# Kernel optimization log

Hardware: AMD Instinct MI355X
Metric: run time of the kernel (lower is better)

## Reference

```python
import jax, jax.numpy as jnp
import numpy as np

N_HEADS = 16
NEG_INF = float('-inf')


def setup_inputs() -> dict:
    key = jax.random.key(0)
    ks = jax.random.split(key, 8)
    B, S, D = 8, 1024, 1024
    inp = {
        'q': jax.random.normal(ks[0], (B, S, D), jnp.float32),
        'k': jax.random.normal(ks[1], (B, S, D), jnp.float32),
        'v': jax.random.normal(ks[2], (B, S, D), jnp.float32),
        'key_padding_mask': jnp.zeros((B, S), bool),
        'Wq': jax.random.normal(ks[3], (D, D), jnp.float32) / np.sqrt(D),
        'bq': jnp.zeros((D,), jnp.float32),
        'Wk': jax.random.normal(ks[4], (D, D), jnp.float32) / np.sqrt(D),
        'bk': jnp.zeros((D,), jnp.float32),
        'Wv': jax.random.normal(ks[5], (D, D), jnp.float32) / np.sqrt(D),
        'bv': jnp.zeros((D,), jnp.float32),
        'Wo': jax.random.normal(ks[6], (D, D), jnp.float32) / np.sqrt(D),
        'bo': jnp.zeros((D,), jnp.float32),
    }
    return inp


def reference(q, k, v, key_padding_mask, Wq, bq, Wk, bk, Wv, bv, Wo, bo):
    B, T, D = q.shape
    S = k.shape[1]
    H = N_HEADS
    dh = D // H
    causal = True

    # projections (torch Linear: x @ W.T + b)
    qh = (q @ Wq.T + bq).reshape(B, T, H, dh).transpose(0, 2, 1, 3)  # b h t d
    kh = (k @ Wk.T + bk).reshape(B, S, H, dh).transpose(0, 2, 1, 3)  # b h s d
    vh = (v @ Wv.T + bv).reshape(B, S, H, dh).transpose(0, 2, 1, 3)  # b h s d

    s = jnp.einsum('bhtd,bhsd->bhts', qh, kh) / jnp.sqrt(jnp.asarray(dh, s_dtype(qh)))
    s = jnp.where(key_padding_mask[:, None, None, :], NEG_INF, s)
    if causal:
        cmask = jnp.triu(jnp.full((T, S), NEG_INF, s.dtype), 1)
        s = s + cmask[None, None]
    a = jax.nn.softmax(s.astype(jnp.float32), axis=-1).astype(s.dtype)
    o = jnp.einsum('bhts,bhsd->bhtd', a, vh)
    o = o.transpose(0, 2, 1, 3).reshape(B, T, D)
    return o @ Wo.T + bo


def s_dtype(x):
    return x.dtype
```

## Files before the change

### kernel.cpp

```cpp
#include <hip/hip_runtime.h>
#include <hip/hip_bf16.h>

typedef unsigned short u16;
typedef unsigned int u32;
typedef __attribute__((ext_vector_type(8))) short bf16x8;
typedef __attribute__((ext_vector_type(4))) float f32x4;

#define LOG2E 1.44269504088896340736f
#define QSCALE (0.125f * LOG2E)
#define DEFER_THR 8.0f


__device__ inline u16 f2bf(float f) {
  union { float f; u32 u; } v; v.f = f;
  u32 r = v.u + 0x7fffu + ((v.u >> 16) & 1u);
  return (u16)(r >> 16);
}

__device__ inline void gload_lds16(const void* g, void* l) {
  __builtin_amdgcn_global_load_lds(
      (const __attribute__((address_space(1))) u32*)g,
      (__attribute__((address_space(3))) u32*)l, 16, 0, 0);
}

template<int CTRL>
__device__ inline float dppmov(float x) {
  int i = __builtin_bit_cast(int, x);
  int r = __builtin_amdgcn_update_dpp(i, i, CTRL, 0xf, 0xf, false);
  return __builtin_bit_cast(float, r);
}
__device__ inline float rowmax16(float v) {
  v = fmaxf(v, dppmov<0x128>(v));
  v = fmaxf(v, dppmov<0x124>(v));
  v = fmaxf(v, dppmov<0x122>(v));
  v = fmaxf(v, dppmov<0x121>(v));
  return v;
}
__device__ inline float rowsum16(float v) {
  v += dppmov<0x128>(v);
  v += dppmov<0x124>(v);
  v += dppmov<0x122>(v);
  v += dppmov<0x121>(v);
  return v;
}


__global__ void cvt_multi(const float4* __restrict__ s0, const float4* __restrict__ s1,
                          const float4* __restrict__ s2, const float4* __restrict__ s3,
                          ushort4* __restrict__ d0, ushort4* __restrict__ d1,
                          ushort4* __restrict__ d2, ushort4* __restrict__ d3, int n4) {
  const float4* s; ushort4* d;
  switch (blockIdx.y) {
    case 0: s = s0; d = d0; break;
    case 1: s = s1; d = d1; break;
    case 2: s = s2; d = d2; break;
    default: s = s3; d = d3; break;
  }
  int stride = gridDim.x * blockDim.x;
  for (int i = blockIdx.x * blockDim.x + threadIdx.x; i < n4; i += stride) {
    float4 v = s[i];
    ushort4 o;
    o.x = f2bf(v.x); o.y = f2bf(v.y); o.z = f2bf(v.z); o.w = f2bf(v.w);
    d[i] = o;
  }
}


__global__ void mask_flags(const unsigned char* __restrict__ mask,
                           unsigned char* __restrict__ flags) {
  int t = threadIdx.x;
  if (t >= 128) return;
  const uint4* p = (const uint4*)(mask + (size_t)t * 64);
  uint4 a = p[0], b = p[1], c = p[2], d = p[3];
  u32 v = a.x | a.y | a.z | a.w | b.x | b.y | b.z | b.w |
          c.x | c.y | c.z | c.w | d.x | d.y | d.z | d.w;
  flags[t] = v ? 1 : 0;
}


#define GATE() do { \
    asm volatile("s_waitcnt vmcnt(4)" ::: "memory"); \
    __builtin_amdgcn_s_barrier(); \
    __builtin_amdgcn_sched_barrier(0); \
  } while (0)

#define READ_A(buf, qm)                                                        \
  do {                                                                         \
    const char* base_ = (const char*)&sA[buf][wm][0];                          \
    _Pragma("unroll")                                                          \
    for (int fi = 0; fi < 4; ++fi) {                                           \
      _Pragma("unroll")                                                        \
      for (int kk = 0; kk < 2; ++kk) {                                         \
        int row_ = (qm) * 64 + fi * 16 + r;                                    \
        int j_ = kk * 4 + g;                                                   \
        af[fi][kk] = *(const bf16x8*)(base_ + row_ * 128 +                     \
                                      ((j_ ^ (row_ & 7)) << 4));               \
      }                                                                        \
    }                                                                          \
  } while (0)

#define READ_B(buf, qn, BF)                                                    \
  do {                                                                         \
    const char* base_ = (const char*)&sB[buf][wn >> 1][0];                     \
    _Pragma("unroll")                                                          \
    for (int fj = 0; fj < 2; ++fj) {                                           \
      _Pragma("unroll")                                                        \
      for (int kk = 0; kk < 2; ++kk) {                                         \
        int row_ = (wn & 1) * 64 + (qn) * 32 + fj * 16 + r;                    \
        int j_ = kk * 4 + g;                                                   \
        BF[fj][kk] = *(const bf16x8*)(base_ + row_ * 128 +                     \
                                      ((j_ ^ (row_ & 7)) << 4));               \
      }                                                                        \
    }                                                                          \
  } while (0)

#define MFMA8(qm, qn, BF)                                                      \
  do {                                                                         \
    __builtin_amdgcn_s_setprio(1);                                             \
    _Pragma("unroll")                                                          \
    for (int kk = 0; kk < 2; ++kk) {                                           \
      _Pragma("unroll")                                                        \
      for (int fi = 0; fi < 4; ++fi) {                                         \
        _Pragma("unroll")                                                      \
        for (int fj = 0; fj < 2; ++fj) {                                       \
          acc[(qm) * 4 + fi][(qn) * 2 + fj] =                                  \
              __builtin_amdgcn_mfma_f32_16x16x32_bf16(                         \
                  af[fi][kk], BF[fj][kk], acc[(qm) * 4 + fi][(qn) * 2 + fj],   \
                  0, 0, 0);                                                    \
        }                                                                      \
      }                                                                        \
    }                                                                          \
    __builtin_amdgcn_s_setprio(0);                                             \
  } while (0)

__global__ __launch_bounds__(512) void gemm_qkv8(
    const u16* __restrict__ Aq, const u16* __restrict__ Ak, const u16* __restrict__ Av,
    const u16* __restrict__ Wqb, const u16* __restrict__ Wkb, const u16* __restrict__ Wvb,
    const float* __restrict__ bqp, const float* __restrict__ bkp, const float* __restrict__ bvp,
    u16* __restrict__ Qh, u16* __restrict__ Kh, u16* __restrict__ Vt,
    int M, int N, int K) {
  __shared__ u16 sA[2][2][128 * 64];
  __shared__ u16 sB[2][2][128 * 64];

  const int hw = blockIdx.z * 128 + blockIdx.y * 4 + blockIdx.x;
  const int lg = (hw & 7) * 48 + (hw >> 3);
  const int z = lg >> 7;
  const int rem = lg & 127;
  const int m0 = (rem >> 2) * 256;
  const int n0 = (rem & 3) * 256;

  const u16* A  = (z == 0) ? Aq : (z == 1) ? Ak : Av;
  const u16* Bt = (z == 0) ? Wqb : (z == 1) ? Wkb : Wvb;
  const float* bias = (z == 0) ? bqp : (z == 1) ? bkp : bvp;

  const int tid = threadIdx.x;
  const int lane = tid & 63;
  const int wave = tid >> 6;
  const int g = lane >> 4;
  const int r = lane & 15;
  const int wm = wave >> 2;
  const int wn = wave & 3;

  f32x4 acc[8][4] = {};
  bf16x8 af[4][2], bf0[2][2], bf1[2][2];

  auto stageA = [&](int buf, int half, int kt) {
    const int k0 = kt * 64;
#pragma unroll
    for (int i = 0; i < 2; ++i) {
      int c = tid + i * 512;
      int row = c >> 3, cc = c & 7;
      gload_lds16(A + (size_t)(m0 + half * 128 + row) * K + k0 + ((cc ^ (row & 7)) * 8),
                  &sA[buf][half][0] + c * 8);
    }
  };
  auto stageB = [&](int buf, int half, int kt) {
    const int k0 = kt * 64;
#pragma unroll
    for (int i = 0; i < 2; ++i) {
      int c = tid + i * 512;
      int row = c >> 3, cc = c & 7;
      gload_lds16(Bt + (size_t)(n0 + half * 128 + row) * K + k0 + ((cc ^ (row & 7)) * 8),
                  &sB[buf][half][0] + c * 8);
    }
  };

  const int NT = K / 64;

  stageB(0, 0, 0); stageB(0, 1, 0); stageA(0, 0, 0); stageA(0, 1, 0);
  stageB(1, 0, 1); stageA(1, 0, 1);
  asm volatile("s_waitcnt vmcnt(0)" ::: "memory");
  __builtin_amdgcn_s_barrier();
  __builtin_amdgcn_sched_barrier(0);

  for (int t = 0; t < NT; ++t) {
    const int buf = t & 1;
    READ_A(buf, 0);
    READ_B(buf, 0, bf0);
    if (t + 1 < NT) stageB(buf ^ 1, 1, t + 1);
    GATE();
    MFMA8(0, 0, bf0);
    READ_B(buf, 1, bf1);
    if (t + 1 < NT) stageA(buf ^ 1, 1, t + 1);
    GATE();
    MFMA8(0, 1, bf1);
    READ_A(buf, 1);
    if (t + 2 < NT) stageB(buf, 0, t + 2);
    GATE();
    MFMA8(1, 0, bf0);
    if (t + 2 < NT) stageA(buf, 0, t + 2);
    GATE();
    MFMA8(1, 1, bf1);
  }

#pragma unroll
  for (int fi = 0; fi < 8; ++fi) {
    int rowb = m0 + wm * 128 + fi * 16 + g * 4;
#pragma unroll
    for (int fj = 0; fj < 4; ++fj) {
      int col = n0 + wn * 64 + fj * 16 + r;
      float bv = bias[col];
#pragma unroll
      for (int q = 0; q < 4; ++q) {
        int row = rowb + q;
        float v = acc[fi][fj][q] + bv;
        int b = row >> 10, t = row & 1023, h = col >> 6, d = col & 63;
        if (z == 0) {
          Qh[((((size_t)b * 16 + h) << 10) + t) * 64 + d] = f2bf(v * QSCALE);
        } else if (z == 1) {
          Kh[((((size_t)b * 16 + h) << 10) + t) * 64 + d] = f2bf(v);
        } else {
          Vt[(((size_t)b * 16 + h) * 64 + d) * 1024 + t] = f2bf(v);
        }
      }
    }
  }
}


__global__ __launch_bounds__(256) void gemm_o(
    const u16* __restrict__ A, const u16* __restrict__ Bt,
    const float* __restrict__ bias, float* __restrict__ Cout,
    int M, int N, int K) {
  constexpr int BK = 32;
  __shared__ u16 sA[2][128 * BK];
  __shared__ u16 sB[2][128 * BK];

  const int hw = blockIdx.y * 8 + blockIdx.x;
  const int lg = (hw & 7) * 64 + (hw >> 3);
  const int m0 = (lg >> 3) * 128;
  const int n0 = (lg & 7) * 128;

  const int tid = threadIdx.x;
  const int lane = tid & 63;
  const int wave = tid >> 6;
  const int g = lane >> 4;
  const int r = lane & 15;
  const int wr = wave >> 1, wc = wave & 1;

  f32x4 acc[4][4] = {};

  auto stage = [&](int buf, int kt) {
    const int k0 = kt * BK;
#pragma unroll
    for (int i = 0; i < 2; ++i) {
      int c = tid + i * 256;
      int row = c >> 2, cc = c & 3;
      gload_lds16(A + (size_t)(m0 + row) * K + k0 + cc * 8, &sA[buf][0] + c * 8);
    }
#pragma unroll
    for (int i = 0; i < 2; ++i) {
      int c = tid + i * 256;
      int row = c >> 2, cc = c & 3;
      gload_lds16(Bt + (size_t)(n0 + row) * K + k0 + cc * 8, &sB[buf][0] + c * 8);
    }
  };

  stage(0, 0);
  const int NT = K / BK;
  for (int kt = 0; kt < NT; ++kt) {
    __syncthreads();
    if (kt + 1 < NT) stage((kt + 1) & 1, kt + 1);
    const u16* a_base = &sA[kt & 1][0];
    const u16* b_base = &sB[kt & 1][0];
    bf16x8 avf[4], bvf[4];
#pragma unroll
    for (int i = 0; i < 4; ++i) {
      avf[i] = *(const bf16x8*)(a_base + (wr * 64 + i * 16 + r) * BK + g * 8);
      bvf[i] = *(const bf16x8*)(b_base + (wc * 64 + i * 16 + r) * BK + g * 8);
    }
#pragma unroll
    for (int i = 0; i < 4; ++i)
#pragma unroll
      for (int j = 0; j < 4; ++j)
        acc[i][j] = __builtin_amdgcn_mfma_f32_16x16x32_bf16(avf[i], bvf[j], acc[i][j], 0, 0, 0);
  }

#pragma unroll
  for (int i = 0; i < 4; ++i) {
    int rowb = m0 + wr * 64 + i * 16 + g * 4;
#pragma unroll
    for (int j = 0; j < 4; ++j) {
      int col = n0 + wc * 64 + j * 16 + r;
      float bv = bias[col];
#pragma unroll
      for (int q = 0; q < 4; ++q) {
        int row = rowb + q;
        Cout[(size_t)row * N + col] = acc[i][j][q] + bv;
      }
    }
  }
}


__global__ __launch_bounds__(256) void attn_fwd(
    const u16* __restrict__ Qh, const u16* __restrict__ Kh,
    const u16* __restrict__ Vt, const unsigned char* __restrict__ mask,
    const unsigned char* __restrict__ padflags,
    u16* __restrict__ O) {
  constexpr int S = 1024, DH = 64;
  __shared__ u16 sK[2][64 * 64];
  __shared__ u16 sV[2][64 * 64];
  __shared__ u16 sP[4][16 * 64];

  const int tid = threadIdx.x, lane = tid & 63, wave = tid >> 6;
  const int g = lane >> 4, r = lane & 15;
  const int bh = blockIdx.x;
  const int qt = (int)gridDim.y - 1 - (int)blockIdx.y;
  const int b = bh >> 4, h = bh & 15;
  const int qw = qt * 128 + wave * 32;

  bf16x8 qf[2][2];
#pragma unroll
  for (int u = 0; u < 2; ++u) {
    const u16* Qb = Qh + ((size_t)bh * S + qw + u * 16 + r) * DH;
    qf[u][0] = *(const bf16x8*)(Qb + g * 8);
    qf[u][1] = *(const bf16x8*)(Qb + 32 + g * 8);
  }

  f32x4 acc[2][4] = {};
  float mrun[2][4], lrun[2][4];
#pragma unroll
  for (int u = 0; u < 2; ++u)
#pragma unroll
    for (int i = 0; i < 4; ++i) { mrun[u][i] = -INFINITY; lrun[u][i] = 0.f; }

  auto stage = [&](int buf, int kvt) {
    const int s0k = kvt * 64;
#pragma unroll
    for (int i = 0; i < 2; ++i) {
      int c = tid + i * 256;
      int row = c >> 3;
      int cc = (c & 7) ^ (row & 7);
      gload_lds16(Kh + ((size_t)bh * S + s0k + row) * DH + cc * 8, &sK[buf][0] + c * 8);
      gload_lds16(Vt + ((size_t)bh * DH + row) * S + s0k + cc * 8, &sV[buf][0] + c * 8);
    }
  };

  const int NT = 2 * (qt + 1);
  stage(0, 0);
  for (int kvt = 0; kvt < NT; ++kvt) {
    __syncthreads();
    if (kvt + 1 < NT) stage((kvt + 1) & 1, kvt + 1);
    const int cur = kvt & 1;
    const int s0 = kvt * 64;
    const bool pad = padflags[b * 16 + (s0 >> 6)] != 0;
    const u16* Kb = &sK[cur][0];
    const u16* Vb = &sV[cur][0];
    u16* Pw = &sP[wave][0];

#pragma unroll
    for (int u = 0; u < 2; ++u) {
      const int qg = qw + u * 16;
      if (s0 > qg + 15) continue;
      const bool diag = (s0 + 63 > qg);

      f32x4 sc[4] = {};
      __builtin_amdgcn_s_setprio(1);
#pragma unroll
      for (int ss = 0; ss < 4; ++ss) {
#pragma unroll
        for (int kc = 0; kc < 2; ++kc) {
          int krow = ss * 16 + r;
          int byteoff = krow * 128 + kc * 64 + g * 16;
          bf16x8 kf = *(const bf16x8*)((const char*)Kb + (byteoff ^ ((krow & 7) << 4)));
          sc[ss] = __builtin_amdgcn_mfma_f32_16x16x32_bf16(qf[u][kc], kf, sc[ss], 0, 0, 0);
        }
      }
      __builtin_amdgcn_s_setprio(0);

      float sv[4][4];
      float pmax[4] = {-INFINITY, -INFINITY, -INFINITY, -INFINITY};
#pragma unroll
      for (int ss = 0; ss < 4; ++ss) {
        float padd = 0.f;
        if (pad) {
          int s_g = s0 + ss * 16 + r;
          if (mask[(size_t)b * S + s_g]) padd = -INFINITY;
        }
#pragma unroll
        for (int reg = 0; reg < 4; ++reg) {
          float v = sc[ss][reg] + padd;
          if (diag) {
            int s_g = s0 + ss * 16 + r;
            int q_g = qg + g * 4 + reg;
            if (s_g > q_g) v = -INFINITY;
          }
          sv[ss][reg] = v;
          pmax[reg] = fmaxf(pmax[reg], v);
        }
      }

      float tm[4];
#pragma unroll
      for (int reg = 0; reg < 4; ++reg) tm[reg] = rowmax16(pmax[reg]);
      float dmax = fmaxf(fmaxf(tm[0] - mrun[u][0], tm[1] - mrun[u][1]),
                         fmaxf(tm[2] - mrun[u][2], tm[3] - mrun[u][3]));
      if (__any(dmax > DEFER_THR)) {
#pragma unroll
        for (int reg = 0; reg < 4; ++reg) {
          float newm = fmaxf(mrun[u][reg], tm[reg]);
          float alpha = (newm == -INFINITY) ? 1.f : exp2f(mrun[u][reg] - newm);
          mrun[u][reg] = newm;
          float rs = 0.f;
#pragma unroll
          for (int ss = 0; ss < 4; ++ss) {
            float p = (newm == -INFINITY) ? 0.f : exp2f(sv[ss][reg] - newm);
            sv[ss][reg] = p;
            rs += p;
          }
          rs = rowsum16(rs);
          lrun[u][reg] = lrun[u][reg] * alpha + rs;
#pragma unroll
          for (int df = 0; df < 4; ++df) acc[u][df][reg] *= alpha;
        }
      } else {
#pragma unroll
        for (int reg = 0; reg < 4; ++reg) {
          float m = mrun[u][reg];
          float rs = 0.f;
#pragma unroll
          for (int ss = 0; ss < 4; ++ss) {
            float p = (m == -INFINITY) ? 0.f : exp2f(sv[ss][reg] - m);
            sv[ss][reg] = p;
            rs += p;
          }
          rs = rowsum16(rs);
          lrun[u][reg] += rs;
        }
      }

#pragma unroll
      for (int ss = 0; ss < 4; ++ss) {
#pragma unroll
        for (int reg = 0; reg < 4; ++reg) {
          int qrow = g * 4 + reg;
          int byteoff = qrow * 128 + (ss * 16 + r) * 2;
          u32 bits = __builtin_bit_cast(u32, sv[ss][reg]);
          *(u16*)((char*)Pw + (byteoff ^ ((qrow & 7) << 4))) = (u16)(bits >> 16);
        }
      }

      __builtin_amdgcn_s_setprio(1);
#pragma unroll
      for (int sc2 = 0; sc2 < 2; ++sc2) {
        int pbyte = r * 128 + sc2 * 64 + g * 16;
        bf16x8 pf = *(const bf16x8*)((const char*)Pw + (pbyte ^ ((r & 7) << 4)));
#pragma unroll
        for (int df = 0; df < 4; ++df) {
          int vrow = df * 16 + r;
          int vbyte = vrow * 128 + sc2 * 64 + g * 16;
          bf16x8 vf = *(const bf16x8*)((const char*)Vb + (vbyte ^ ((vrow & 7) << 4)));
          acc[u][df] = __builtin_amdgcn_mfma_f32_16x16x32_bf16(pf, vf, acc[u][df], 0, 0, 0);
        }
      }
      __builtin_amdgcn_s_setprio(0);
    }
  }

#pragma unroll
  for (int u = 0; u < 2; ++u) {
#pragma unroll
    for (int reg = 0; reg < 4; ++reg) {
      float l = lrun[u][reg];
      float inv = (l > 0.f) ? 1.f / l : 0.f;
      int t = qw + u * 16 + g * 4 + reg;
#pragma unroll
      for (int df = 0; df < 4; ++df) {
        float vo = acc[u][df][reg] * inv;
        O[((size_t)b * 1024 + t) * 1024 + h * 64 + df * 16 + r] = f2bf(vo);
      }
    }
  }
}


extern "C" void kernel_launch(void* const* d_in, const int* in_sizes, int n_in,
                              void* d_out, int out_size, void* d_ws, size_t ws_size,
                              hipStream_t stream) {
  const float* q  = (const float*)d_in[0];
  const float* k  = (const float*)d_in[1];
  const float* v  = (const float*)d_in[2];
  const unsigned char* mask = (const unsigned char*)d_in[3];
  const float* Wq = (const float*)d_in[4];
  const float* bq = (const float*)d_in[5];
  const float* Wk = (const float*)d_in[6];
  const float* bk = (const float*)d_in[7];
  const float* Wv = (const float*)d_in[8];
  const float* bv = (const float*)d_in[9];
  const float* Wo = (const float*)d_in[10];
  const float* bo = (const float*)d_in[11];

  const int M = 8192, N = 1024, K = 1024;
  const size_t MB = 1u << 20;
  char* ws = (char*)d_ws;

  u16* Aq   = (u16*)(ws);
  u16* Ak   = (u16*)(ws + 16 * MB);
  u16* Av   = (u16*)(ws + 32 * MB);
  u16* Qh   = (u16*)(ws + 48 * MB);
  u16* Kh   = (u16*)(ws + 64 * MB);
  u16* Vt   = (u16*)(ws + 80 * MB);
  u16* Wqb  = (u16*)(ws + 96 * MB);
  u16* Wkb  = Wqb + (1u << 20);
  u16* Wvb  = Wkb + (1u << 20);
  u16* Wob  = Wvb + (1u << 20);
  unsigned char* flags = (unsigned char*)(ws + 104 * MB);
  u16* AttO = Aq;

  cvt_multi<<<dim3(1024, 3), 256, 0, stream>>>(
      (const float4*)q, (const float4*)k, (const float4*)v, (const float4*)q,
      (ushort4*)Aq, (ushort4*)Ak, (ushort4*)Av, (ushort4*)Aq, (M * K) / 4);
  cvt_multi<<<dim3(256, 4), 256, 0, stream>>>(
      (const float4*)Wq, (const float4*)Wk, (const float4*)Wv, (const float4*)Wo,
      (ushort4*)Wqb, (ushort4*)Wkb, (ushort4*)Wvb, (ushort4*)Wob, (N * K) / 4);
  mask_flags<<<1, 128, 0, stream>>>(mask, flags);

  gemm_qkv8<<<dim3(4, 32, 3), 512, 0, stream>>>(
      Aq, Ak, Av, Wqb, Wkb, Wvb, bq, bk, bv, Qh, Kh, Vt, M, N, K);

  attn_fwd<<<dim3(128, 8), 256, 0, stream>>>(Qh, Kh, Vt, mask, flags, AttO);

  gemm_o<<<dim3(8, 64), 256, 0, stream>>>(
      AttO, Wob, bo, (float*)d_out, M, N, K);
}
```

Before: 241.5 us.

## Shrink QKV GEMM tile to 256x128 and merge conversion launches

The QKV projection GEMM tile shrinks from 256x256 to 256x128. Its eight waves are rearranged as 4x2, each owning a 64x64 sub-tile, and the grid doubles to 768 blocks for better occupancy and fewer partial waves across the CUs. The vmcnt waits are moved so there is one explicit wait per k-step instead of a wait at every barrier. The activation and weight fp32-to-bf16 conversion kernels are merged into a single launch. In exchange, each tile reuses its A data less, and the reworked wait counts risk race conditions if the outstanding-load accounting is off.

```diff
diff --git a/kernel.cpp b/kernel.cpp
--- a/kernel.cpp
+++ b/kernel.cpp
@@ -45,22 +45,30 @@
 }
 
 
-__global__ void cvt_multi(const float4* __restrict__ s0, const float4* __restrict__ s1,
-                          const float4* __restrict__ s2, const float4* __restrict__ s3,
-                          ushort4* __restrict__ d0, ushort4* __restrict__ d1,
-                          ushort4* __restrict__ d2, ushort4* __restrict__ d3, int n4) {
-  const float4* s; ushort4* d;
+__global__ void cvt_all(const float4* __restrict__ q, const float4* __restrict__ k,
+                        const float4* __restrict__ v,
+                        const float4* __restrict__ Wq, const float4* __restrict__ Wk,
+                        const float4* __restrict__ Wv, const float4* __restrict__ Wo,
+                        ushort4* __restrict__ dq, ushort4* __restrict__ dk,
+                        ushort4* __restrict__ dv,
+                        ushort4* __restrict__ dWq, ushort4* __restrict__ dWk,
+                        ushort4* __restrict__ dWv, ushort4* __restrict__ dWo,
+                        int n4A, int n4W) {
+  const float4* s; ushort4* d; int n4;
   switch (blockIdx.y) {
-    case 0: s = s0; d = d0; break;
-    case 1: s = s1; d = d1; break;
-    case 2: s = s2; d = d2; break;
-    default: s = s3; d = d3; break;
+    case 0: s = q;  d = dq;  n4 = n4A; break;
+    case 1: s = k;  d = dk;  n4 = n4A; break;
+    case 2: s = v;  d = dv;  n4 = n4A; break;
+    case 3: s = Wq; d = dWq; n4 = n4W; break;
+    case 4: s = Wk; d = dWk; n4 = n4W; break;
+    case 5: s = Wv; d = dWv; n4 = n4W; break;
+    default: s = Wo; d = dWo; n4 = n4W; break;
   }
   int stride = gridDim.x * blockDim.x;
   for (int i = blockIdx.x * blockDim.x + threadIdx.x; i < n4; i += stride) {
-    float4 v = s[i];
+    float4 x = s[i];
     ushort4 o;
-    o.x = f2bf(v.x); o.y = f2bf(v.y); o.z = f2bf(v.z); o.w = f2bf(v.w);
+    o.x = f2bf(x.x); o.y = f2bf(x.y); o.z = f2bf(x.z); o.w = f2bf(x.w);
     d[i] = o;
   }
 }
@@ -78,54 +86,53 @@
 }
 
 
-#define GATE() do { \
-    asm volatile("s_waitcnt vmcnt(4)" ::: "memory"); \
+#define BAR8() do { \
     __builtin_amdgcn_s_barrier(); \
     __builtin_amdgcn_sched_barrier(0); \
   } while (0)
 
-#define READ_A(buf, qm)                                                        \
+#define READ_A8(buf, qm)                                                       \
   do {                                                                         \
-    const char* base_ = (const char*)&sA[buf][wm][0];                          \
+    const char* ab_ = (const char*)&sA[buf][wm >> 1][0];                       \
     _Pragma("unroll")                                                          \
-    for (int fi = 0; fi < 4; ++fi) {                                           \
+    for (int fi = 0; fi < 2; ++fi) {                                           \
       _Pragma("unroll")                                                        \
       for (int kk = 0; kk < 2; ++kk) {                                         \
-        int row_ = (qm) * 64 + fi * 16 + r;                                    \
+        int row_ = (wm & 1) * 64 + (qm) * 32 + fi * 16 + r;                    \
         int j_ = kk * 4 + g;                                                   \
-        af[fi][kk] = *(const bf16x8*)(base_ + row_ * 128 +                     \
+        af[fi][kk] = *(const bf16x8*)(ab_ + row_ * 128 +                       \
                                       ((j_ ^ (row_ & 7)) << 4));               \
       }                                                                        \
     }                                                                          \
   } while (0)
 
-#define READ_B(buf, qn, BF)                                                    \
+#define READ_B8(buf, qn, BF)                                                   \
   do {                                                                         \
-    const char* base_ = (const char*)&sB[buf][wn >> 1][0];                     \
+    const char* bb_ = (const char*)&sB[buf][wn][0];                            \
     _Pragma("unroll")                                                          \
     for (int fj = 0; fj < 2; ++fj) {                                           \
       _Pragma("unroll")                                                        \
       for (int kk = 0; kk < 2; ++kk) {                                         \
-        int row_ = (wn & 1) * 64 + (qn) * 32 + fj * 16 + r;                    \
+        int row_ = (qn) * 32 + fj * 16 + r;                                    \
         int j_ = kk * 4 + g;                                                   \
-        BF[fj][kk] = *(const bf16x8*)(base_ + row_ * 128 +                     \
+        BF[fj][kk] = *(const bf16x8*)(bb_ + row_ * 128 +                       \
                                       ((j_ ^ (row_ & 7)) << 4));               \
       }                                                                        \
     }                                                                          \
   } while (0)
 
-#define MFMA8(qm, qn, BF)                                                      \
+#define MFMA8B(qm, qn, BF)                                                     \
   do {                                                                         \
     __builtin_amdgcn_s_setprio(1);                                             \
     _Pragma("unroll")                                                          \
     for (int kk = 0; kk < 2; ++kk) {                                           \
       _Pragma("unroll")                                                        \
-      for (int fi = 0; fi < 4; ++fi) {                                         \
+      for (int fi = 0; fi < 2; ++fi) {                                         \
         _Pragma("unroll")                                                      \
         for (int fj = 0; fj < 2; ++fj) {                                       \
-          acc[(qm) * 4 + fi][(qn) * 2 + fj] =                                  \
+          acc[(qm) * 2 + fi][(qn) * 2 + fj] =                                  \
               __builtin_amdgcn_mfma_f32_16x16x32_bf16(                         \
-                  af[fi][kk], BF[fj][kk], acc[(qm) * 4 + fi][(qn) * 2 + fj],   \
+                  af[fi][kk], BF[fj][kk], acc[(qm) * 2 + fi][(qn) * 2 + fj],   \
                   0, 0, 0);                                                    \
         }                                                                      \
       }                                                                        \
@@ -133,21 +140,21 @@
     __builtin_amdgcn_s_setprio(0);                                             \
   } while (0)
 
-__global__ __launch_bounds__(512) void gemm_qkv8(
+__global__ __launch_bounds__(512) void gemm_qkv8b(
     const u16* __restrict__ Aq, const u16* __restrict__ Ak, const u16* __restrict__ Av,
     const u16* __restrict__ Wqb, const u16* __restrict__ Wkb, const u16* __restrict__ Wvb,
     const float* __restrict__ bqp, const float* __restrict__ bkp, const float* __restrict__ bvp,
     u16* __restrict__ Qh, u16* __restrict__ Kh, u16* __restrict__ Vt,
     int M, int N, int K) {
   __shared__ u16 sA[2][2][128 * 64];
-  __shared__ u16 sB[2][2][128 * 64];
-
-  const int hw = blockIdx.z * 128 + blockIdx.y * 4 + blockIdx.x;
-  const int lg = (hw & 7) * 48 + (hw >> 3);
-  const int z = lg >> 7;
-  const int rem = lg & 127;
-  const int m0 = (rem >> 2) * 256;
-  const int n0 = (rem & 3) * 256;
+  __shared__ u16 sB[2][2][64 * 64];
+
+  const int hw = blockIdx.z * 256 + blockIdx.y * 8 + blockIdx.x;
+  const int lg = (hw & 7) * 96 + (hw >> 3);
+  const int z = lg >> 8;
+  const int rem = lg & 255;
+  const int m0 = (rem >> 3) * 256;
+  const int n0 = (rem & 7) * 128;
 
   const u16* A  = (z == 0) ? Aq : (z == 1) ? Ak : Av;
   const u16* Bt = (z == 0) ? Wqb : (z == 1) ? Wkb : Wvb;
@@ -158,11 +165,11 @@
   const int wave = tid >> 6;
   const int g = lane >> 4;
   const int r = lane & 15;
-  const int wm = wave >> 2;
-  const int wn = wave & 3;
-
-  f32x4 acc[8][4] = {};
-  bf16x8 af[4][2], bf0[2][2], bf1[2][2];
+  const int wm = wave >> 1;
+  const int wn = wave & 1;
+
+  f32x4 acc[4][4] = {};
+  bf16x8 af[2][2], bf0[2][2], bf1[2][2];
 
   auto stageA = [&](int buf, int half, int kt) {
     const int k0 = kt * 64;
@@ -176,46 +183,47 @@
   };
   auto stageB = [&](int buf, int half, int kt) {
     const int k0 = kt * 64;
-#pragma unroll
-    for (int i = 0; i < 2; ++i) {
-      int c = tid + i * 512;
-      int row = c >> 3, cc = c & 7;
-      gload_lds16(Bt + (size_t)(n0 + half * 128 + row) * K + k0 + ((cc ^ (row & 7)) * 8),
-                  &sB[buf][half][0] + c * 8);
-    }
+    int c = tid;
+    int row = c >> 3, cc = c & 7;
+    gload_lds16(Bt + (size_t)(n0 + half * 64 + row) * K + k0 + ((cc ^ (row & 7)) * 8),
+                &sB[buf][half][0] + c * 8);
   };
 
   const int NT = K / 64;
 
   stageB(0, 0, 0); stageB(0, 1, 0); stageA(0, 0, 0); stageA(0, 1, 0);
   stageB(1, 0, 1); stageA(1, 0, 1);
-  asm volatile("s_waitcnt vmcnt(0)" ::: "memory");
-  __builtin_amdgcn_s_barrier();
-  __builtin_amdgcn_sched_barrier(0);
+  asm volatile("s_waitcnt vmcnt(3)" ::: "memory");
+  BAR8();
 
   for (int t = 0; t < NT; ++t) {
     const int buf = t & 1;
-    READ_A(buf, 0);
-    READ_B(buf, 0, bf0);
+    READ_A8(buf, 0);
+    READ_B8(buf, 0, bf0);
     if (t + 1 < NT) stageB(buf ^ 1, 1, t + 1);
-    GATE();
-    MFMA8(0, 0, bf0);
-    READ_B(buf, 1, bf1);
+    BAR8();
+    MFMA8B(0, 0, bf0);
+    READ_B8(buf, 1, bf1);
     if (t + 1 < NT) stageA(buf ^ 1, 1, t + 1);
-    GATE();
-    MFMA8(0, 1, bf1);
-    READ_A(buf, 1);
+    BAR8();
+    MFMA8B(0, 1, bf1);
+    READ_A8(buf, 1);
     if (t + 2 < NT) stageB(buf, 0, t + 2);
-    GATE();
-    MFMA8(1, 0, bf0);
-    if (t + 2 < NT) stageA(buf, 0, t + 2);
-    GATE();
-    MFMA8(1, 1, bf1);
-  }
-
-#pragma unroll
-  for (int fi = 0; fi < 8; ++fi) {
-    int rowb = m0 + wm * 128 + fi * 16 + g * 4;
+    BAR8();
+    MFMA8B(1, 0, bf0);
+    if (t + 2 < NT) {
+      stageA(buf, 0, t + 2);
+      asm volatile("s_waitcnt vmcnt(3)" ::: "memory");
+    } else if (t + 1 < NT) {
+      asm volatile("s_waitcnt vmcnt(0)" ::: "memory");
+    }
+    BAR8();
+    MFMA8B(1, 1, bf1);
+  }
+
+#pragma unroll
+  for (int fi = 0; fi < 4; ++fi) {
+    int rowb = m0 + wm * 64 + fi * 16 + g * 4;
 #pragma unroll
     for (int fj = 0; fj < 4; ++fj) {
       int col = n0 + wn * 64 + fj * 16 + r;
@@ -528,15 +536,15 @@
   unsigned char* flags = (unsigned char*)(ws + 104 * MB);
   u16* AttO = Aq;
 
-  cvt_multi<<<dim3(1024, 3), 256, 0, stream>>>(
-      (const float4*)q, (const float4*)k, (const float4*)v, (const float4*)q,
-      (ushort4*)Aq, (ushort4*)Ak, (ushort4*)Av, (ushort4*)Aq, (M * K) / 4);
-  cvt_multi<<<dim3(256, 4), 256, 0, stream>>>(
+  cvt_all<<<dim3(1024, 7), 256, 0, stream>>>(
+      (const float4*)q, (const float4*)k, (const float4*)v,
       (const float4*)Wq, (const float4*)Wk, (const float4*)Wv, (const float4*)Wo,
-      (ushort4*)Wqb, (ushort4*)Wkb, (ushort4*)Wvb, (ushort4*)Wob, (N * K) / 4);
+      (ushort4*)Aq, (ushort4*)Ak, (ushort4*)Av,
+      (ushort4*)Wqb, (ushort4*)Wkb, (ushort4*)Wvb, (ushort4*)Wob,
+      (M * K) / 4, (N * K) / 4);
   mask_flags<<<1, 128, 0, stream>>>(mask, flags);
 
-  gemm_qkv8<<<dim3(4, 32, 3), 512, 0, stream>>>(
+  gemm_qkv8b<<<dim3(8, 32, 3), 512, 0, stream>>>(
       Aq, Ak, Av, Wqb, Wkb, Wvb, bq, bk, bv, Qh, Kh, Vt, M, N, K);
 
   attn_fwd<<<dim3(128, 8), 256, 0, stream>>>(Qh, Kh, Vt, mask, flags, AttO);
```

Measured after the change: 241.1 us. About the same (-0.2%).
